# Kernel tuning notes

Hardware: AMD Instinct MI355X
Metric: run time of the kernel (lower is better)

The kernel has to match this reference:

```python
import jax, jax.numpy as jnp
import numpy as np
import math

DIM_PER_HEAD = 64

def setup_inputs() -> dict:
    key = jax.random.key(0)
    k1, k2, k3, k4 = jax.random.split(key, 4)
    B, H, S, D = 2, 16, 2048, 64
    mat1 = jax.random.normal(k1, (B, H, S, D), dtype=jnp.float32)
    mat2 = jax.random.normal(k2, (B, H, S, D), dtype=jnp.float32)
    mat3 = jax.random.normal(k3, (B, H, S, D), dtype=jnp.float32)
    bias = jax.random.normal(k4, (1, 1, S, S), dtype=jnp.float32)
    return {"mat1": mat1, "mat2": mat2, "mat3": mat3, "bias": bias}

def reference(mat1, mat2, mat3, bias) -> jnp.ndarray:
    # scale Q, scores = QK^T + bias, softmax over last dim, then @ V
    scale = 1.0 / math.sqrt(DIM_PER_HEAD)
    qk = jnp.einsum('bhqd,bhkd->bhqk', mat1 * scale, mat2)  # [B,H,S,S]
    scores = jax.nn.softmax(qk + bias, axis=-1)
    return jnp.einsum('bhqk,bhkd->bhqd', scores, mat3)
```

## Files before the change

### kernel.cpp

```cpp
#include <hip/hip_runtime.h>
#include <hip/hip_bf16.h>


#define SEQ 2048
#define DH  64
#define BHN 32
#define LOG2E 1.44269504088896f

typedef __attribute__((ext_vector_type(8))) short bf16x8;
typedef __attribute__((ext_vector_type(4))) float f32x4;
typedef __attribute__((ext_vector_type(8))) short short8v;

__device__ inline short f2b(float x) {
    union { float f; unsigned u; } v; v.f = x;
    unsigned r = v.u + 0x7fff + ((v.u >> 16) & 1);
    return (short)(r >> 16);
}

__device__ inline void gl_lds16(const void* g, void* l) {
    __builtin_amdgcn_global_load_lds(
        (const __attribute__((address_space(1))) void*)g,
        (__attribute__((address_space(3))) void*)l, 16, 0, 0);
}

__device__ __host__ inline int phi(int r) {
    return 32 * (r >> 5) + 16 * ((r >> 2) & 1) + 4 * ((r >> 3) & 3) + (r & 3);
}

__global__ __launch_bounds__(256)
void prep_kv(const float* __restrict__ K, const float* __restrict__ V,
             short* __restrict__ Kb, short* __restrict__ Vt) {
    __shared__ short t[64 * 72];
    const int tid = threadIdx.x;
    const int bh = blockIdx.x >> 5, st = blockIdx.x & 31, s0 = st * 64;

    {
        const float* Kp = K + ((size_t)bh * SEQ + s0) * DH;
        short* Ko = Kb + ((size_t)bh * SEQ + s0) * DH;
        #pragma unroll
        for (int i = 0; i < 2; ++i) {
            size_t o = (size_t)(tid + i * 256) * 8;
            f32x4 a = *(const f32x4*)(Kp + o);
            f32x4 b = *(const f32x4*)(Kp + o + 4);
            short8v s;
            #pragma unroll
            for (int j = 0; j < 4; ++j) { s[j] = f2b(a[j]); s[4 + j] = f2b(b[j]); }
            *(short8v*)(Ko + o) = s;
        }
    }

    const float* Vb = V + (size_t)bh * SEQ * DH + (size_t)s0 * DH;
    #pragma unroll
    for (int i = 0; i < 4; ++i) {
        int c = tid + i * 256, s = c >> 4, c4 = c & 15;
        f32x4 v = *(const f32x4*)(Vb + s * DH + c4 * 4);
        #pragma unroll
        for (int j = 0; j < 4; ++j) t[s * 72 + c4 * 4 + j] = f2b(v[j]);
    }
    __syncthreads();
    const int d = tid >> 2, part = tid & 3;
    short* outp = Vt + (size_t)bh * DH * SEQ + (size_t)d * SEQ + s0 + part * 16;
    #pragma unroll
    for (int h = 0; h < 2; ++h) {
        short8v w;
        #pragma unroll
        for (int u = 0; u < 8; ++u) {
            int rho = part * 16 + h * 8 + u;
            w[u] = t[phi(rho) * 72 + d];
        }
        *(short8v*)(outp + h * 8) = w;
    }
}

__global__ __launch_bounds__(256, 4)
void mha_main(const float* __restrict__ Q, const float* __restrict__ Bias,
              const short* __restrict__ Kb, const short* __restrict__ Vt,
              float* __restrict__ Out)
{
    __shared__ short kA[64 * DH];
    __shared__ short kB[64 * DH];
    __shared__ short vA[64 * DH];
    __shared__ short vB[64 * DH];

    const int tid = threadIdx.x, lane = tid & 63, wave = tid >> 6;
    const int l15 = lane & 15, l4 = lane >> 4;
    const int qb = blockIdx.x & 31, bh = blockIdx.x >> 5;
    const int q0 = qb * 64;

    const float* Qb = Q + (size_t)bh * SEQ * DH;
    const short* Kh = Kb + (size_t)bh * SEQ * DH;
    const short* Vh = Vt + (size_t)bh * DH * SEQ;
    float* Ob = Out + (size_t)bh * SEQ * DH;

    bf16x8 qf[2];
    {
        const float* qp = Qb + (size_t)(q0 + wave * 16 + l15) * DH;
        #pragma unroll
        for (int ks = 0; ks < 2; ++ks) {
            short tmp[8];
            #pragma unroll
            for (int j = 0; j < 8; ++j) tmp[j] = f2b(qp[ks * 32 + l4 * 8 + j] * (0.125f * LOG2E));
            qf[ks] = *reinterpret_cast<bf16x8*>(tmp);
        }
    }

    f32x4 o_acc[4];
    #pragma unroll
    for (int dt = 0; dt < 4; ++dt) o_acc[dt] = f32x4{0.f, 0.f, 0.f, 0.f};
    float l_part = 0.f;

    const short *kg0, *kg1, *vg0, *vg1;
    int off0, off1;
    {
        int s0_ = wave * 64 + lane, r0 = s0_ >> 3, c0 = s0_ & 7, g0 = c0 ^ (r0 & 7);
        int s1_ = 256 + wave * 64 + lane, r1 = s1_ >> 3, c1 = s1_ & 7, g1 = c1 ^ (r1 & 7);
        kg0 = Kh + (size_t)r0 * DH + g0 * 8;
        vg0 = Vh + (size_t)r0 * SEQ + g0 * 8;
        kg1 = Kh + (size_t)r1 * DH + g1 * 8;
        vg1 = Vh + (size_t)r1 * SEQ + g1 * 8;
        off0 = (wave * 64) * 8;
        off1 = (256 + wave * 64) * 8;
    }
    const float* bp0 = Bias + (size_t)(q0 + wave * 16 + l15) * SEQ + l4 * 4;
    const int swz = l15 & 7;

    gl_lds16(kg0, kA + off0);
    gl_lds16(kg1, kA + off1);
    gl_lds16(vg0, vA + off0);
    gl_lds16(vg1, vA + off1);
    f32x4 bv[4];
    #pragma unroll
    for (int nt = 0; nt < 4; ++nt)
        bv[nt] = *(const f32x4*)(bp0 + nt * 16);

    auto body = [&](int kt, const short* kc, const short* vc,
                    short* knx, short* vnx) {
        __syncthreads();

        bf16x8 kfr[2][4];
        #pragma unroll
        for (int ks = 0; ks < 2; ++ks)
            #pragma unroll
            for (int nt = 0; nt < 4; ++nt) {
                int cc = (ks * 4 + l4) ^ swz;
                kfr[ks][nt] = *(const bf16x8*)&kc[(nt * 16 + l15) * DH + cc * 8];
            }
        bf16x8 vfr[2][4];
        #pragma unroll
        for (int ks = 0; ks < 2; ++ks)
            #pragma unroll
            for (int dt = 0; dt < 4; ++dt) {
                int cc = (ks * 4 + l4) ^ swz;
                vfr[ks][dt] = *(const bf16x8*)&vc[(dt * 16 + l15) * DH + cc * 8];
            }

        const int kn = (kt + 1) & 31;
        gl_lds16(kg0 + (size_t)kn * 64 * DH, knx + off0);
        gl_lds16(kg1 + (size_t)kn * 64 * DH, knx + off1);
        gl_lds16(vg0 + kn * 64, vnx + off0);
        gl_lds16(vg1 + kn * 64, vnx + off1);

        f32x4 sacc[4];
        #pragma unroll
        for (int nt = 0; nt < 4; ++nt) sacc[nt] = f32x4{0.f, 0.f, 0.f, 0.f};
        #pragma unroll
        for (int ks = 0; ks < 2; ++ks)
            #pragma unroll
            for (int nt = 0; nt < 4; ++nt)
                sacc[nt] = __builtin_amdgcn_mfma_f32_16x16x32_bf16(kfr[ks][nt], qf[ks], sacc[nt], 0, 0, 0);

        unsigned pk[4][2];
        #pragma unroll
        for (int nt = 0; nt < 4; ++nt) {
            float pv[4];
            #pragma unroll
            for (int r = 0; r < 4; ++r) {
                pv[r] = __builtin_amdgcn_exp2f(__builtin_fmaf(bv[nt][r], LOG2E, sacc[nt][r]));
                l_part += pv[r];
            }
            #pragma unroll
            for (int rp = 0; rp < 2; ++rp) {
                __hip_bfloat162 h2 = __float22bfloat162_rn(float2{pv[2 * rp], pv[2 * rp + 1]});
                pk[nt][rp] = *reinterpret_cast<unsigned*>(&h2);
            }
        }

        {
            const float* bp = bp0 + kn * 64;
            #pragma unroll
            for (int nt = 0; nt < 4; ++nt)
                bv[nt] = *(const f32x4*)(bp + nt * 16);
        }

        #pragma unroll
        for (int ks = 0; ks < 2; ++ks) {
            union { bf16x8 v; unsigned u[4]; } af;
            af.u[0] = pk[2 * ks][0]; af.u[1] = pk[2 * ks][1];
            af.u[2] = pk[2 * ks + 1][0]; af.u[3] = pk[2 * ks + 1][1];
            #pragma unroll
            for (int dt = 0; dt < 4; ++dt)
                o_acc[dt] = __builtin_amdgcn_mfma_f32_16x16x32_bf16(af.v, vfr[ks][dt], o_acc[dt], 0, 0, 0);
        }
    };

    for (int kt = 0; kt < SEQ / 64; kt += 2) {
        body(kt,     kA, vA, kB, vB);
        body(kt + 1, kB, vB, kA, vA);
    }

    l_part += __shfl_xor(l_part, 16, 64);
    l_part += __shfl_xor(l_part, 32, 64);

    #pragma unroll
    for (int r = 0; r < 4; ++r) {
        float lr = __shfl(l_part, l4 * 4 + r, 64);
        float inv = 1.0f / lr;
        float* op = Ob + (size_t)(q0 + wave * 16 + l4 * 4 + r) * DH + l15;
        #pragma unroll
        for (int dt = 0; dt < 4; ++dt) op[dt * 16] = o_acc[dt][r] * inv;
    }
}

extern "C" void kernel_launch(void* const* d_in, const int* in_sizes, int n_in,
                              void* d_out, int out_size, void* d_ws, size_t ws_size,
                              hipStream_t stream) {
    const float* Q    = (const float*)d_in[0];
    const float* K    = (const float*)d_in[1];
    const float* V    = (const float*)d_in[2];
    const float* Bias = (const float*)d_in[3];
    float* O          = (float*)d_out;

    short* Kb = (short*)d_ws;
    short* Vt = Kb + (size_t)BHN * SEQ * DH;

    prep_kv<<<dim3(BHN * 32), dim3(256), 0, stream>>>(K, V, Kb, Vt);
    mha_main<<<dim3(BHN * 32), dim3(256), 0, stream>>>(Q, Bias, Kb, Vt, O);
}
```

Measured before the change: 184.0 us.

## Process two 16-row query groups per wave to reuse K/V fragments

Each wave now handles 32 query rows (two groups of 16) instead of 16, so a block covers 128 queries and the grid is halved. The K and V fragments read from LDS, and the K/V tile staging, are amortised over twice as many MFMAs, which cuts LDS and global K/V traffic per query. In exchange register pressure roughly doubles for accumulators and bias, so launch bounds drop to 2 blocks per SM. Only 512 blocks are launched, which may underfill the GPU's compute units.

```diff
diff --git a/kernel.cpp b/kernel.cpp
--- a/kernel.cpp
+++ b/kernel.cpp
@@ -72,7 +72,7 @@
     }
 }
 
-__global__ __launch_bounds__(256, 4)
+__global__ __launch_bounds__(256, 2)
 void mha_main(const float* __restrict__ Q, const float* __restrict__ Bias,
               const short* __restrict__ Kb, const short* __restrict__ Vt,
               float* __restrict__ Out)
@@ -84,30 +84,33 @@
 
     const int tid = threadIdx.x, lane = tid & 63, wave = tid >> 6;
     const int l15 = lane & 15, l4 = lane >> 4;
-    const int qb = blockIdx.x & 31, bh = blockIdx.x >> 5;
-    const int q0 = qb * 64;
+    const int qb = blockIdx.x & 15, bh = blockIdx.x >> 4;
+    const int q0 = qb * 128;
 
     const float* Qb = Q + (size_t)bh * SEQ * DH;
     const short* Kh = Kb + (size_t)bh * SEQ * DH;
     const short* Vh = Vt + (size_t)bh * DH * SEQ;
     float* Ob = Out + (size_t)bh * SEQ * DH;
 
-    bf16x8 qf[2];
-    {
-        const float* qp = Qb + (size_t)(q0 + wave * 16 + l15) * DH;
+    bf16x8 qf[2][2];
+    #pragma unroll
+    for (int g = 0; g < 2; ++g) {
+        const float* qp = Qb + (size_t)(q0 + wave * 32 + g * 16 + l15) * DH;
         #pragma unroll
         for (int ks = 0; ks < 2; ++ks) {
             short tmp[8];
             #pragma unroll
             for (int j = 0; j < 8; ++j) tmp[j] = f2b(qp[ks * 32 + l4 * 8 + j] * (0.125f * LOG2E));
-            qf[ks] = *reinterpret_cast<bf16x8*>(tmp);
-        }
-    }
-
-    f32x4 o_acc[4];
-    #pragma unroll
-    for (int dt = 0; dt < 4; ++dt) o_acc[dt] = f32x4{0.f, 0.f, 0.f, 0.f};
-    float l_part = 0.f;
+            qf[g][ks] = *reinterpret_cast<bf16x8*>(tmp);
+        }
+    }
+
+    f32x4 o_acc[2][4];
+    #pragma unroll
+    for (int g = 0; g < 2; ++g)
+        #pragma unroll
+        for (int dt = 0; dt < 4; ++dt) o_acc[g][dt] = f32x4{0.f, 0.f, 0.f, 0.f};
+    float l_part[2] = {0.f, 0.f};
 
     const short *kg0, *kg1, *vg0, *vg1;
     int off0, off1;
@@ -121,17 +124,22 @@
         off0 = (wave * 64) * 8;
         off1 = (256 + wave * 64) * 8;
     }
-    const float* bp0 = Bias + (size_t)(q0 + wave * 16 + l15) * SEQ + l4 * 4;
+    const float* bpg[2];
+    #pragma unroll
+    for (int g = 0; g < 2; ++g)
+        bpg[g] = Bias + (size_t)(q0 + wave * 32 + g * 16 + l15) * SEQ + l4 * 4;
     const int swz = l15 & 7;
 
     gl_lds16(kg0, kA + off0);
     gl_lds16(kg1, kA + off1);
     gl_lds16(vg0, vA + off0);
     gl_lds16(vg1, vA + off1);
-    f32x4 bv[4];
-    #pragma unroll
-    for (int nt = 0; nt < 4; ++nt)
-        bv[nt] = *(const f32x4*)(bp0 + nt * 16);
+    f32x4 bv[2][4];
+    #pragma unroll
+    for (int g = 0; g < 2; ++g)
+        #pragma unroll
+        for (int nt = 0; nt < 4; ++nt)
+            bv[g][nt] = *(const f32x4*)(bpg[g] + nt * 16);
 
     auto body = [&](int kt, const short* kc, const short* vc,
                     short* knx, short* vnx) {
@@ -160,47 +168,58 @@
         gl_lds16(vg0 + kn * 64, vnx + off0);
         gl_lds16(vg1 + kn * 64, vnx + off1);
 
-        f32x4 sacc[4];
-        #pragma unroll
-        for (int nt = 0; nt < 4; ++nt) sacc[nt] = f32x4{0.f, 0.f, 0.f, 0.f};
+        f32x4 sacc[2][4];
+        #pragma unroll
+        for (int g = 0; g < 2; ++g)
+            #pragma unroll
+            for (int nt = 0; nt < 4; ++nt) sacc[g][nt] = f32x4{0.f, 0.f, 0.f, 0.f};
         #pragma unroll
         for (int ks = 0; ks < 2; ++ks)
             #pragma unroll
             for (int nt = 0; nt < 4; ++nt)
-                sacc[nt] = __builtin_amdgcn_mfma_f32_16x16x32_bf16(kfr[ks][nt], qf[ks], sacc[nt], 0, 0, 0);
-
-        unsigned pk[4][2];
-        #pragma unroll
-        for (int nt = 0; nt < 4; ++nt) {
-            float pv[4];
-            #pragma unroll
-            for (int r = 0; r < 4; ++r) {
-                pv[r] = __builtin_amdgcn_exp2f(__builtin_fmaf(bv[nt][r], LOG2E, sacc[nt][r]));
-                l_part += pv[r];
-            }
-            #pragma unroll
-            for (int rp = 0; rp < 2; ++rp) {
-                __hip_bfloat162 h2 = __float22bfloat162_rn(float2{pv[2 * rp], pv[2 * rp + 1]});
-                pk[nt][rp] = *reinterpret_cast<unsigned*>(&h2);
-            }
-        }
-
-        {
-            const float* bp = bp0 + kn * 64;
+                #pragma unroll
+                for (int g = 0; g < 2; ++g)
+                    sacc[g][nt] = __builtin_amdgcn_mfma_f32_16x16x32_bf16(
+                        kfr[ks][nt], qf[g][ks], sacc[g][nt], 0, 0, 0);
+
+        unsigned pk[2][4][2];
+        #pragma unroll
+        for (int g = 0; g < 2; ++g)
+            #pragma unroll
+            for (int nt = 0; nt < 4; ++nt) {
+                float pv[4];
+                #pragma unroll
+                for (int r = 0; r < 4; ++r) {
+                    pv[r] = __builtin_amdgcn_exp2f(__builtin_fmaf(bv[g][nt][r], LOG2E, sacc[g][nt][r]));
+                    l_part[g] += pv[r];
+                }
+                #pragma unroll
+                for (int rp = 0; rp < 2; ++rp) {
+                    __hip_bfloat162 h2 = __float22bfloat162_rn(float2{pv[2 * rp], pv[2 * rp + 1]});
+                    pk[g][nt][rp] = *reinterpret_cast<unsigned*>(&h2);
+                }
+            }
+
+        #pragma unroll
+        for (int g = 0; g < 2; ++g) {
+            const float* bp = bpg[g] + kn * 64;
             #pragma unroll
             for (int nt = 0; nt < 4; ++nt)
-                bv[nt] = *(const f32x4*)(bp + nt * 16);
-        }
-
-        #pragma unroll
-        for (int ks = 0; ks < 2; ++ks) {
-            union { bf16x8 v; unsigned u[4]; } af;
-            af.u[0] = pk[2 * ks][0]; af.u[1] = pk[2 * ks][1];
-            af.u[2] = pk[2 * ks + 1][0]; af.u[3] = pk[2 * ks + 1][1];
-            #pragma unroll
-            for (int dt = 0; dt < 4; ++dt)
-                o_acc[dt] = __builtin_amdgcn_mfma_f32_16x16x32_bf16(af.v, vfr[ks][dt], o_acc[dt], 0, 0, 0);
-        }
+                bv[g][nt] = *(const f32x4*)(bp + nt * 16);
+        }
+
+        #pragma unroll
+        for (int ks = 0; ks < 2; ++ks)
+            #pragma unroll
+            for (int g = 0; g < 2; ++g) {
+                union { bf16x8 v; unsigned u[4]; } af;
+                af.u[0] = pk[g][2 * ks][0];     af.u[1] = pk[g][2 * ks][1];
+                af.u[2] = pk[g][2 * ks + 1][0]; af.u[3] = pk[g][2 * ks + 1][1];
+                #pragma unroll
+                for (int dt = 0; dt < 4; ++dt)
+                    o_acc[g][dt] = __builtin_amdgcn_mfma_f32_16x16x32_bf16(
+                        af.v, vfr[ks][dt], o_acc[g][dt], 0, 0, 0);
+            }
     };
 
     for (int kt = 0; kt < SEQ / 64; kt += 2) {
@@ -208,16 +227,19 @@
         body(kt + 1, kB, vB, kA, vA);
     }
 
-    l_part += __shfl_xor(l_part, 16, 64);
-    l_part += __shfl_xor(l_part, 32, 64);
-
-    #pragma unroll
-    for (int r = 0; r < 4; ++r) {
-        float lr = __shfl(l_part, l4 * 4 + r, 64);
-        float inv = 1.0f / lr;
-        float* op = Ob + (size_t)(q0 + wave * 16 + l4 * 4 + r) * DH + l15;
-        #pragma unroll
-        for (int dt = 0; dt < 4; ++dt) op[dt * 16] = o_acc[dt][r] * inv;
+    #pragma unroll
+    for (int g = 0; g < 2; ++g) {
+        float s = l_part[g];
+        s += __shfl_xor(s, 16, 64);
+        s += __shfl_xor(s, 32, 64);
+        #pragma unroll
+        for (int r = 0; r < 4; ++r) {
+            float lr = __shfl(s, l4 * 4 + r, 64);
+            float inv = 1.0f / lr;
+            float* op = Ob + (size_t)(q0 + wave * 32 + g * 16 + l4 * 4 + r) * DH + l15;
+            #pragma unroll
+            for (int dt = 0; dt < 4; ++dt) op[dt * 16] = o_acc[g][dt][r] * inv;
+        }
     }
 }
 
@@ -234,5 +256,5 @@
     short* Vt = Kb + (size_t)BHN * SEQ * DH;
 
     prep_kv<<<dim3(BHN * 32), dim3(256), 0, stream>>>(K, V, Kb, Vt);
-    mha_main<<<dim3(BHN * 32), dim3(256), 0, stream>>>(Q, Bias, Kb, Vt, O);
-}
+    mha_main<<<dim3(BHN * 16), dim3(256), 0, stream>>>(Q, Bias, Kb, Vt, O);
+}
```

Result: faster. 171.2 us (-6.9%).
